# Optimization experiments

Measured on AMD Instinct MI355X. Metric: run time of the kernel, lower is better.

The kernel has to match this reference:

```python
import jax, jax.numpy as jnp
import numpy as np

B, S, D = 2, 2048, 1024
H = 16
DH = D // H  # 64

def setup_inputs() -> dict:
    key = jax.random.key(0)
    ks = jax.random.split(key, 7)
    sc = 1.0 / np.sqrt(DH)
    return {
        "sequences": jax.random.normal(ks[0], (B, S, D), dtype=jnp.float32),
        "Wq": jax.random.normal(ks[1], (H, DH, DH), dtype=jnp.float32) * sc,
        "bq": jax.random.normal(ks[2], (H, DH), dtype=jnp.float32) * 0.02,
        "Wk": jax.random.normal(ks[3], (H, DH, DH), dtype=jnp.float32) * sc,
        "bk": jax.random.normal(ks[4], (H, DH), dtype=jnp.float32) * 0.02,
        "Wv": jax.random.normal(ks[5], (H, DH, DH), dtype=jnp.float32) * sc,
        "bv": jax.random.normal(ks[6], (H, DH), dtype=jnp.float32) * 0.02,
    }

def reference(sequences, Wq, bq, Wk, bk, Wv, bv):
    b, s, _ = sequences.shape
    x = sequences.reshape(b, s, H, DH)  # [B,S,H,Dh]
    # torch Linear: y = x @ W^T + b; W is [out,in] => einsum contracts input dim d
    q = jnp.einsum("bshd,hed->bshe", x, Wq) + bq  # [B,S,H,Dh]
    k = jnp.einsum("bshd,hed->bshe", x, Wk) + bk
    v = jnp.einsum("bshd,hed->bshe", x, Wv) + bv
    scores = jnp.einsum("bshd,bthd->bhst", q, k) / jnp.sqrt(jnp.float32(DH))
    attn = jax.nn.softmax(scores, axis=-1)  # [B,H,S,S]
    out = jnp.einsum("bhst,bthd->bshd", attn, v)  # [B,S,H,Dh]
    return out.reshape(b, s, H * DH)
```

## Files before the change

kernel.cpp:

```cpp
#include <hip/hip_runtime.h>

typedef unsigned short u16;
typedef __bf16 bf16x8 __attribute__((ext_vector_type(8)));
typedef float  f32x4  __attribute__((ext_vector_type(4)));
typedef u16    u16x4  __attribute__((ext_vector_type(4)));

#define HH   16
#define DHH  64
#define SEQL 2048
#define NB   2
#define BHN  (NB * HH)

static __device__ __forceinline__ u16 f2bf(float f) {
    return __builtin_bit_cast(u16, (__bf16)f);
}

static __device__ __forceinline__ void gload_lds16(const void* g, void* l) {
    __builtin_amdgcn_global_load_lds(
        (const __attribute__((address_space(1))) unsigned int*)g,
        (__attribute__((address_space(3))) unsigned int*)l, 16, 0, 0);
}

__global__ __launch_bounds__(256) void wconv_kernel(
    const float* __restrict__ Wq, const float* __restrict__ Wk,
    const float* __restrict__ Wv, u16* __restrict__ Wb)
{
    const int m = blockIdx.y;
    const float* W = (m == 0) ? Wq : (m == 1) ? Wk : Wv;
    const int i = (blockIdx.x * 256 + threadIdx.x) * 4;
    float4 v = *reinterpret_cast<const float4*>(W + i);
    u16x4 o = { f2bf(v.x), f2bf(v.y), f2bf(v.z), f2bf(v.w) };
    *reinterpret_cast<u16x4*>(Wb + (size_t)m * 65536 + i) = o;
}

__global__ __launch_bounds__(256) void qkv_kernel(
    const float* __restrict__ x, const u16* __restrict__ Wb,
    const float* __restrict__ bq, const float* __restrict__ bk,
    const float* __restrict__ bv,
    u16* __restrict__ Qws, u16* __restrict__ Kws, u16* __restrict__ Vtws)
{
    const int h   = blockIdx.y;
    const int r0  = blockIdx.x * 64;
    const int tid = threadIdx.x;
    const int w   = tid >> 6;
    const int l   = tid & 63;
    const int c   = l & 15;
    const int g   = l >> 4;

    __shared__ u16 vt[64 * 72];

    bf16x8 xa[2];
    {
        const float* xp = x + (size_t)(r0 + w * 16 + c) * 1024 + h * 64 + g * 8;
        #pragma unroll
        for (int kh = 0; kh < 2; ++kh) {
            float4 lo = *reinterpret_cast<const float4*>(xp + kh * 32);
            float4 hi = *reinterpret_cast<const float4*>(xp + kh * 32 + 4);
            bf16x8 f;
            f[0]=(__bf16)lo.x; f[1]=(__bf16)lo.y; f[2]=(__bf16)lo.z; f[3]=(__bf16)lo.w;
            f[4]=(__bf16)hi.x; f[5]=(__bf16)hi.y; f[6]=(__bf16)hi.z; f[7]=(__bf16)hi.w;
            xa[kh] = f;
        }
    }

    const int b      = r0 >> 11;
    const int s_base = r0 & (SEQL - 1);
    const int bh     = b * HH + h;

    const float* bs[3] = {bq + h * 64, bk + h * 64, bv + h * 64};

    #pragma unroll
    for (int m = 0; m < 3; ++m) {
        const u16*   W    = Wb + (size_t)m * 65536 + h * 4096;
        const float* bias = bs[m];
        f32x4 acc[4];
        #pragma unroll
        for (int ct = 0; ct < 4; ++ct) {
            acc[ct][0] = 0.f; acc[ct][1] = 0.f; acc[ct][2] = 0.f; acc[ct][3] = 0.f;
        }
        #pragma unroll
        for (int kh = 0; kh < 2; ++kh) {
            #pragma unroll
            for (int ct = 0; ct < 4; ++ct) {
                bf16x8 wf = *reinterpret_cast<const bf16x8*>(
                    W + (ct * 16 + c) * 64 + kh * 32 + g * 8);
                acc[ct] = __builtin_amdgcn_mfma_f32_16x16x32_bf16(xa[kh], wf, acc[ct], 0, 0, 0);
            }
        }
        if (m < 2) {
            u16* outp = (m == 0 ? Qws : Kws) +
                        ((size_t)bh * SEQL + s_base + w * 16 + g * 4) * 64;
            #pragma unroll
            for (int ct = 0; ct < 4; ++ct) {
                float bb = bias[ct * 16 + c];
                #pragma unroll
                for (int r = 0; r < 4; ++r)
                    outp[(size_t)r * 64 + ct * 16 + c] = f2bf(acc[ct][r] + bb);
            }
        } else {
            #pragma unroll
            for (int ct = 0; ct < 4; ++ct) {
                float bb = bias[ct * 16 + c];
                u16x4 pb;
                #pragma unroll
                for (int r = 0; r < 4; ++r)
                    pb[r] = f2bf(acc[ct][r] + bb);
                *reinterpret_cast<u16x4*>(&vt[(ct * 16 + c) * 72 + w * 16 + g * 4]) = pb;
            }
        }
    }
    __syncthreads();
    {
        const int d  = tid >> 2;
        const int s0 = (tid & 3) * 16;
        u16* vp = Vtws + ((size_t)bh * 64 + d) * SEQL + s_base + s0;
        uint4 v0 = *reinterpret_cast<const uint4*>(&vt[d * 72 + s0]);
        uint4 v1 = *reinterpret_cast<const uint4*>(&vt[d * 72 + s0 + 8]);
        *reinterpret_cast<uint4*>(vp)     = v0;
        *reinterpret_cast<uint4*>(vp + 8) = v1;
    }
}

__global__ __launch_bounds__(256) void attn_kernel(
    const u16* __restrict__ Qws, const u16* __restrict__ Kws,
    const u16* __restrict__ Vtws, float* __restrict__ out)
{
    const int p     = blockIdx.x;
    const int lid   = (p & 7) * 64 + (p >> 3);
    const int qtile = lid & 15;
    const int bh    = lid >> 4;
    const int b     = bh >> 4;
    const int h     = bh & 15;

    const int tid = threadIdx.x;
    const int w   = tid >> 6;
    const int l   = tid & 63;
    const int c   = l & 15;
    const int g   = l >> 4;
    const int q0  = qtile * 128 + w * 32;

    __shared__ u16 k_lds[2][64 * 64];
    __shared__ u16 v_lds[2][64 * 64];
    __shared__ u16 plds_all[4 * 32 * 64];
    char* pbase = reinterpret_cast<char*>(plds_all + w * (32 * 64));

    const u16* Kb = Kws  + (size_t)bh * SEQL * 64;
    const u16* Vb = Vtws + (size_t)bh * 64 * SEQL;

    const int rs8 = l >> 3;
    const int sx  = (l & 7) ^ rs8;

    #define STAGE(bb, k0)                                                     \
    {   _Pragma("unroll")                                                     \
        for (int a = 0; a < 2; ++a) {                                         \
            const int rbase = w * 16 + a * 8;                                 \
            const int r     = rbase + rs8;                                    \
            gload_lds16(Kb + (size_t)((k0) + r) * 64 + sx * 8,                \
                        &k_lds[bb][rbase * 64]);                              \
            gload_lds16(Vb + (size_t)r * SEQL + (k0) + sx * 8,                \
                        &v_lds[bb][rbase * 64]);                              \
        }                                                                     \
    }

    bf16x8 qf[2][2];
    #pragma unroll
    for (int qt = 0; qt < 2; ++qt)
        #pragma unroll
        for (int kh = 0; kh < 2; ++kh)
            qf[qt][kh] = *reinterpret_cast<const bf16x8*>(
                Qws + ((size_t)bh * SEQL + q0 + qt * 16 + c) * 64 + kh * 32 + g * 8);

    const f32x4 zero4 = {0.f, 0.f, 0.f, 0.f};
    bf16x8 ones8;
    #pragma unroll
    for (int j = 0; j < 8; ++j) ones8[j] = __builtin_bit_cast(__bf16, (u16)0x3F80);

    f32x4 acc[4][2];
    #pragma unroll
    for (int dt = 0; dt < 4; ++dt)
        #pragma unroll
        for (int qt = 0; qt < 2; ++qt) acc[dt][qt] = zero4;
    float mrow[2] = {-1e30f, -1e30f};
    float lrow[2] = {0.f, 0.f};
    const float SCL = 0.125f * 1.44269504088896340736f;

    const int rdoff = ((g ^ (c & 7)) * 8);

    STAGE(0, 0);
    __syncthreads();

    for (int t = 0; t < SEQL / 64; ++t) {
        const int cur = t & 1;

        if (t + 1 < SEQL / 64) STAGE(cur ^ 1, (t + 1) * 64);

        f32x4 st[4][2];
        __builtin_amdgcn_s_setprio(1);
        #pragma unroll
        for (int kt = 0; kt < 4; ++kt) {
            const int e0 = (kt * 16 + c) * 64 + rdoff;
            bf16x8 ka0 = *reinterpret_cast<const bf16x8*>(&k_lds[cur][e0]);
            bf16x8 ka1 = *reinterpret_cast<const bf16x8*>(&k_lds[cur][e0 ^ 32]);
            #pragma unroll
            for (int qt = 0; qt < 2; ++qt) {
                st[kt][qt] = __builtin_amdgcn_mfma_f32_16x16x32_bf16(ka0, qf[qt][0], zero4,      0, 0, 0);
                st[kt][qt] = __builtin_amdgcn_mfma_f32_16x16x32_bf16(ka1, qf[qt][1], st[kt][qt], 0, 0, 0);
            }
        }
        __builtin_amdgcn_s_setprio(0);

        bf16x8 vf[8];
        #pragma unroll
        for (int dt = 0; dt < 4; ++dt) {
            const int e0 = (dt * 16 + c) * 64 + rdoff;
            vf[dt * 2]     = *reinterpret_cast<const bf16x8*>(&v_lds[cur][e0]);
            vf[dt * 2 + 1] = *reinterpret_cast<const bf16x8*>(&v_lds[cur][e0 ^ 32]);
        }

        #pragma unroll
        for (int qt = 0; qt < 2; ++qt) {
            float a0 = fmaxf(st[0][qt][0], st[0][qt][1]);
            float a1 = fmaxf(st[0][qt][2], st[0][qt][3]);
            float a2 = fmaxf(st[1][qt][0], st[1][qt][1]);
            float a3 = fmaxf(st[1][qt][2], st[1][qt][3]);
            float a4 = fmaxf(st[2][qt][0], st[2][qt][1]);
            float a5 = fmaxf(st[2][qt][2], st[2][qt][3]);
            float a6 = fmaxf(st[3][qt][0], st[3][qt][1]);
            float a7 = fmaxf(st[3][qt][2], st[3][qt][3]);
            float b0 = fmaxf(fmaxf(a0, a1), fmaxf(a2, a3));
            float b1 = fmaxf(fmaxf(a4, a5), fmaxf(a6, a7));
            float mx = fmaxf(b0, b1);
            mx = fmaxf(mx, __shfl_xor(mx, 16, 64));
            mx = fmaxf(mx, __shfl_xor(mx, 32, 64));
            const float mx_s = mx * SCL;

            if (!__all(mx_s <= mrow[qt] + 8.f)) {
                const float mn    = fmaxf(mrow[qt], mx_s);
                const float alpha = __builtin_amdgcn_exp2f(mrow[qt] - mn);
                mrow[qt] = mn;
                lrow[qt] *= alpha;
                #pragma unroll
                for (int dt = 0; dt < 4; ++dt) {
                    acc[dt][qt][0] *= alpha; acc[dt][qt][1] *= alpha;
                    acc[dt][qt][2] *= alpha; acc[dt][qt][3] *= alpha;
                }
            }

            const int row = qt * 16 + c;
            #pragma unroll
            for (int kt = 0; kt < 4; ++kt) {
                u16x4 pb;
                #pragma unroll
                for (int r = 0; r < 4; ++r)
                    pb[r] = f2bf(__builtin_amdgcn_exp2f(fmaf(st[kt][qt][r], SCL, -mrow[qt])));
                const int blk = (kt * 2 + (g >> 1)) ^ (row & 7);
                *reinterpret_cast<u16x4*>(pbase + row * 128 + blk * 16 + (g & 1) * 8) = pb;
            }
        }

        asm volatile("s_waitcnt lgkmcnt(0)" ::: "memory");

        bf16x8 pf[2][2];
        #pragma unroll
        for (int qt = 0; qt < 2; ++qt) {
            const int row = qt * 16 + c;
            #pragma unroll
            for (int kh = 0; kh < 2; ++kh) {
                const int blk = (kh * 4 + g) ^ (row & 7);
                pf[qt][kh] = *reinterpret_cast<const bf16x8*>(pbase + row * 128 + blk * 16);
            }
        }

        __builtin_amdgcn_s_setprio(1);
        #pragma unroll
        for (int dt = 0; dt < 4; ++dt) {
            #pragma unroll
            for (int qt = 0; qt < 2; ++qt) {
                acc[dt][qt] = __builtin_amdgcn_mfma_f32_16x16x32_bf16(vf[dt*2],   pf[qt][0], acc[dt][qt], 0, 0, 0);
                acc[dt][qt] = __builtin_amdgcn_mfma_f32_16x16x32_bf16(vf[dt*2+1], pf[qt][1], acc[dt][qt], 0, 0, 0);
            }
        }
        f32x4 su[2];
        #pragma unroll
        for (int qt = 0; qt < 2; ++qt) {
            su[qt] = __builtin_amdgcn_mfma_f32_16x16x32_bf16(ones8, pf[qt][0], zero4,   0, 0, 0);
            su[qt] = __builtin_amdgcn_mfma_f32_16x16x32_bf16(ones8, pf[qt][1], su[qt], 0, 0, 0);
        }
        __builtin_amdgcn_s_setprio(0);
        lrow[0] += su[0][0];
        lrow[1] += su[1][0];

        __syncthreads();
    }

    const float inv0 = 1.f / lrow[0];
    const float inv1 = 1.f / lrow[1];
    #pragma unroll
    for (int qt = 0; qt < 2; ++qt) {
        const float inv = qt ? inv1 : inv0;
        float* op = out + ((size_t)b * SEQL + q0 + qt * 16 + c) * 1024 + h * 64 + g * 4;
        #pragma unroll
        for (int dt = 0; dt < 4; ++dt) {
            float4 o;
            o.x = acc[dt][qt][0] * inv; o.y = acc[dt][qt][1] * inv;
            o.z = acc[dt][qt][2] * inv; o.w = acc[dt][qt][3] * inv;
            *reinterpret_cast<float4*>(op + dt * 16) = o;
        }
    }
}

extern "C" void kernel_launch(void* const* d_in, const int* in_sizes, int n_in,
                              void* d_out, int out_size, void* d_ws, size_t ws_size,
                              hipStream_t stream) {
    const float* x  = (const float*)d_in[0];
    const float* Wq = (const float*)d_in[1];
    const float* bq = (const float*)d_in[2];
    const float* Wk = (const float*)d_in[3];
    const float* bk = (const float*)d_in[4];
    const float* Wv = (const float*)d_in[5];
    const float* bv = (const float*)d_in[6];
    float* out = (float*)d_out;

    const size_t per = (size_t)BHN * SEQL * 64;
    u16* Qws = (u16*)d_ws;
    u16* Kws = Qws + per;
    u16* Vt  = Kws + per;
    u16* Wb  = Vt  + per;

    wconv_kernel<<<dim3(64, 3), 256, 0, stream>>>(Wq, Wk, Wv, Wb);
    qkv_kernel<<<dim3(64, 16), 256, 0, stream>>>(x, Wb, bq, bk, bv, Qws, Kws, Vt);
    attn_kernel<<<dim3(512), 256, 0, stream>>>(Qws, Kws, Vt, out);
}
```

Baseline: 89.23 us.

## Halve attention query tile to 64 rows per block and double grid

Each wave now handles 16 query rows instead of 32, so a block covers 64 queries and the grid grows from 512 to 1024 blocks. This roughly halves accumulator and score register use and improves load balance and occupancy across the CUs. The cost is that K/V tiles are reloaded from global memory twice as often per query, giving less reuse per LDS stage and more total traffic.

Measured after the change: 92.66 us. 3.8% more time.

```diff
diff --git a/kernel.cpp b/kernel.cpp
--- a/kernel.cpp
+++ b/kernel.cpp
@@ -126,9 +126,9 @@
     const u16* __restrict__ Vtws, float* __restrict__ out)
 {
     const int p     = blockIdx.x;
-    const int lid   = (p & 7) * 64 + (p >> 3);
-    const int qtile = lid & 15;
-    const int bh    = lid >> 4;
+    const int lid   = (p & 7) * 128 + (p >> 3);
+    const int qtile = lid & 31;
+    const int bh    = lid >> 5;
     const int b     = bh >> 4;
     const int h     = bh & 15;
 
@@ -137,12 +137,12 @@
     const int l   = tid & 63;
     const int c   = l & 15;
     const int g   = l >> 4;
-    const int q0  = qtile * 128 + w * 32;
+    const int q0  = qtile * 64 + w * 16;
 
     __shared__ u16 k_lds[2][64 * 64];
     __shared__ u16 v_lds[2][64 * 64];
-    __shared__ u16 plds_all[4 * 32 * 64];
-    char* pbase = reinterpret_cast<char*>(plds_all + w * (32 * 64));
+    __shared__ u16 plds_all[4 * 16 * 64];
+    char* pbase = reinterpret_cast<char*>(plds_all + w * (16 * 64));
 
     const u16* Kb = Kws  + (size_t)bh * SEQL * 64;
     const u16* Vb = Vtws + (size_t)bh * 64 * SEQL;
@@ -162,26 +162,22 @@
         }                                                                     \
     }
 
-    bf16x8 qf[2][2];
-    #pragma unroll
-    for (int qt = 0; qt < 2; ++qt)
-        #pragma unroll
-        for (int kh = 0; kh < 2; ++kh)
-            qf[qt][kh] = *reinterpret_cast<const bf16x8*>(
-                Qws + ((size_t)bh * SEQL + q0 + qt * 16 + c) * 64 + kh * 32 + g * 8);
+    bf16x8 qf[2];
+    #pragma unroll
+    for (int kh = 0; kh < 2; ++kh)
+        qf[kh] = *reinterpret_cast<const bf16x8*>(
+            Qws + ((size_t)bh * SEQL + q0 + c) * 64 + kh * 32 + g * 8);
 
     const f32x4 zero4 = {0.f, 0.f, 0.f, 0.f};
     bf16x8 ones8;
     #pragma unroll
     for (int j = 0; j < 8; ++j) ones8[j] = __builtin_bit_cast(__bf16, (u16)0x3F80);
 
-    f32x4 acc[4][2];
-    #pragma unroll
-    for (int dt = 0; dt < 4; ++dt)
-        #pragma unroll
-        for (int qt = 0; qt < 2; ++qt) acc[dt][qt] = zero4;
-    float mrow[2] = {-1e30f, -1e30f};
-    float lrow[2] = {0.f, 0.f};
+    f32x4 acc[4];
+    #pragma unroll
+    for (int dt = 0; dt < 4; ++dt) acc[dt] = zero4;
+    float mrow = -1e30f;
+    float lrow = 0.f;
     const float SCL = 0.125f * 1.44269504088896340736f;
 
     const int rdoff = ((g ^ (c & 7)) * 8);
@@ -194,18 +190,15 @@
 
         if (t + 1 < SEQL / 64) STAGE(cur ^ 1, (t + 1) * 64);
 
-        f32x4 st[4][2];
+        f32x4 st[4];
         __builtin_amdgcn_s_setprio(1);
         #pragma unroll
         for (int kt = 0; kt < 4; ++kt) {
             const int e0 = (kt * 16 + c) * 64 + rdoff;
             bf16x8 ka0 = *reinterpret_cast<const bf16x8*>(&k_lds[cur][e0]);
             bf16x8 ka1 = *reinterpret_cast<const bf16x8*>(&k_lds[cur][e0 ^ 32]);
-            #pragma unroll
-            for (int qt = 0; qt < 2; ++qt) {
-                st[kt][qt] = __builtin_amdgcn_mfma_f32_16x16x32_bf16(ka0, qf[qt][0], zero4,      0, 0, 0);
-                st[kt][qt] = __builtin_amdgcn_mfma_f32_16x16x32_bf16(ka1, qf[qt][1], st[kt][qt], 0, 0, 0);
-            }
+            st[kt] = __builtin_amdgcn_mfma_f32_16x16x32_bf16(ka0, qf[0], zero4,  0, 0, 0);
+            st[kt] = __builtin_amdgcn_mfma_f32_16x16x32_bf16(ka1, qf[1], st[kt], 0, 0, 0);
         }
         __builtin_amdgcn_s_setprio(0);
 
@@ -217,16 +210,15 @@
             vf[dt * 2 + 1] = *reinterpret_cast<const bf16x8*>(&v_lds[cur][e0 ^ 32]);
         }
 
-        #pragma unroll
-        for (int qt = 0; qt < 2; ++qt) {
-            float a0 = fmaxf(st[0][qt][0], st[0][qt][1]);
-            float a1 = fmaxf(st[0][qt][2], st[0][qt][3]);
-            float a2 = fmaxf(st[1][qt][0], st[1][qt][1]);
-            float a3 = fmaxf(st[1][qt][2], st[1][qt][3]);
-            float a4 = fmaxf(st[2][qt][0], st[2][qt][1]);
-            float a5 = fmaxf(st[2][qt][2], st[2][qt][3]);
-            float a6 = fmaxf(st[3][qt][0], st[3][qt][1]);
-            float a7 = fmaxf(st[3][qt][2], st[3][qt][3]);
+        {
+            float a0 = fmaxf(st[0][0], st[0][1]);
+            float a1 = fmaxf(st[0][2], st[0][3]);
+            float a2 = fmaxf(st[1][0], st[1][1]);
+            float a3 = fmaxf(st[1][2], st[1][3]);
+            float a4 = fmaxf(st[2][0], st[2][1]);
+            float a5 = fmaxf(st[2][2], st[2][3]);
+            float a6 = fmaxf(st[3][0], st[3][1]);
+            float a7 = fmaxf(st[3][2], st[3][3]);
             float b0 = fmaxf(fmaxf(a0, a1), fmaxf(a2, a3));
             float b1 = fmaxf(fmaxf(a4, a5), fmaxf(a6, a7));
             float mx = fmaxf(b0, b1);
@@ -234,78 +226,61 @@
             mx = fmaxf(mx, __shfl_xor(mx, 32, 64));
             const float mx_s = mx * SCL;
 
-            if (!__all(mx_s <= mrow[qt] + 8.f)) {
-                const float mn    = fmaxf(mrow[qt], mx_s);
-                const float alpha = __builtin_amdgcn_exp2f(mrow[qt] - mn);
-                mrow[qt] = mn;
-                lrow[qt] *= alpha;
+            if (!__all(mx_s <= mrow + 8.f)) {
+                const float mn    = fmaxf(mrow, mx_s);
+                const float alpha = __builtin_amdgcn_exp2f(mrow - mn);
+                mrow = mn;
+                lrow *= alpha;
                 #pragma unroll
                 for (int dt = 0; dt < 4; ++dt) {
-                    acc[dt][qt][0] *= alpha; acc[dt][qt][1] *= alpha;
-                    acc[dt][qt][2] *= alpha; acc[dt][qt][3] *= alpha;
+                    acc[dt][0] *= alpha; acc[dt][1] *= alpha;
+                    acc[dt][2] *= alpha; acc[dt][3] *= alpha;
                 }
             }
 
-            const int row = qt * 16 + c;
             #pragma unroll
             for (int kt = 0; kt < 4; ++kt) {
                 u16x4 pb;
                 #pragma unroll
                 for (int r = 0; r < 4; ++r)
-                    pb[r] = f2bf(__builtin_amdgcn_exp2f(fmaf(st[kt][qt][r], SCL, -mrow[qt])));
-                const int blk = (kt * 2 + (g >> 1)) ^ (row & 7);
-                *reinterpret_cast<u16x4*>(pbase + row * 128 + blk * 16 + (g & 1) * 8) = pb;
+                    pb[r] = f2bf(__builtin_amdgcn_exp2f(fmaf(st[kt][r], SCL, -mrow)));
+                const int blk = (kt * 2 + (g >> 1)) ^ (c & 7);
+                *reinterpret_cast<u16x4*>(pbase + c * 128 + blk * 16 + (g & 1) * 8) = pb;
             }
         }
 
         asm volatile("s_waitcnt lgkmcnt(0)" ::: "memory");
 
-        bf16x8 pf[2][2];
-        #pragma unroll
-        for (int qt = 0; qt < 2; ++qt) {
-            const int row = qt * 16 + c;
-            #pragma unroll
-            for (int kh = 0; kh < 2; ++kh) {
-                const int blk = (kh * 4 + g) ^ (row & 7);
-                pf[qt][kh] = *reinterpret_cast<const bf16x8*>(pbase + row * 128 + blk * 16);
-            }
+        bf16x8 pf[2];
+        #pragma unroll
+        for (int kh = 0; kh < 2; ++kh) {
+            const int blk = (kh * 4 + g) ^ (c & 7);
+            pf[kh] = *reinterpret_cast<const bf16x8*>(pbase + c * 128 + blk * 16);
         }
 
         __builtin_amdgcn_s_setprio(1);
         #pragma unroll
         for (int dt = 0; dt < 4; ++dt) {
-            #pragma unroll
-            for (int qt = 0; qt < 2; ++qt) {
-                acc[dt][qt] = __builtin_amdgcn_mfma_f32_16x16x32_bf16(vf[dt*2],   pf[qt][0], acc[dt][qt], 0, 0, 0);
-                acc[dt][qt] = __builtin_amdgcn_mfma_f32_16x16x32_bf16(vf[dt*2+1], pf[qt][1], acc[dt][qt], 0, 0, 0);
-            }
-        }
-        f32x4 su[2];
-        #pragma unroll
-        for (int qt = 0; qt < 2; ++qt) {
-            su[qt] = __builtin_amdgcn_mfma_f32_16x16x32_bf16(ones8, pf[qt][0], zero4,   0, 0, 0);
-            su[qt] = __builtin_amdgcn_mfma_f32_16x16x32_bf16(ones8, pf[qt][1], su[qt], 0, 0, 0);
-        }
+            acc[dt] = __builtin_amdgcn_mfma_f32_16x16x32_bf16(vf[dt*2],   pf[0], acc[dt], 0, 0, 0);
+            acc[dt] = __builtin_amdgcn_mfma_f32_16x16x32_bf16(vf[dt*2+1], pf[1], acc[dt], 0, 0, 0);
+        }
+        f32x4 su;
+        su = __builtin_amdgcn_mfma_f32_16x16x32_bf16(ones8, pf[0], zero4, 0, 0, 0);
+        su = __builtin_amdgcn_mfma_f32_16x16x32_bf16(ones8, pf[1], su,    0, 0, 0);
         __builtin_amdgcn_s_setprio(0);
-        lrow[0] += su[0][0];
-        lrow[1] += su[1][0];
+        lrow += su[0];
 
         __syncthreads();
     }
 
-    const float inv0 = 1.f / lrow[0];
-    const float inv1 = 1.f / lrow[1];
-    #pragma unroll
-    for (int qt = 0; qt < 2; ++qt) {
-        const float inv = qt ? inv1 : inv0;
-        float* op = out + ((size_t)b * SEQL + q0 + qt * 16 + c) * 1024 + h * 64 + g * 4;
-        #pragma unroll
-        for (int dt = 0; dt < 4; ++dt) {
-            float4 o;
-            o.x = acc[dt][qt][0] * inv; o.y = acc[dt][qt][1] * inv;
-            o.z = acc[dt][qt][2] * inv; o.w = acc[dt][qt][3] * inv;
-            *reinterpret_cast<float4*>(op + dt * 16) = o;
-        }
+    const float inv = 1.f / lrow;
+    float* op = out + ((size_t)b * SEQL + q0 + c) * 1024 + h * 64 + g * 4;
+    #pragma unroll
+    for (int dt = 0; dt < 4; ++dt) {
+        float4 o;
+        o.x = acc[dt][0] * inv; o.y = acc[dt][1] * inv;
+        o.z = acc[dt][2] * inv; o.w = acc[dt][3] * inv;
+        *reinterpret_cast<float4*>(op + dt * 16) = o;
     }
 }
 
@@ -329,5 +304,5 @@
 
     wconv_kernel<<<dim3(64, 3), 256, 0, stream>>>(Wq, Wk, Wv, Wb);
     qkv_kernel<<<dim3(64, 16), 256, 0, stream>>>(x, Wb, bq, bk, bv, Qws, Kws, Vt);
-    attn_kernel<<<dim3(512), 256, 0, stream>>>(Qws, Kws, Vt, out);
-}
+    attn_kernel<<<dim3(1024), 256, 0, stream>>>(Qws, Kws, Vt, out);
+}
```

## Software-pipeline PV MFMA behind next QK tile and fold softmax scale into Wq

Applied to the files above, without the earlier changes.

The P·V matrix multiplies for tile t-1 now run right after the QK^T multiplies for tile t. This is done with double-buffered V and P register fragments, so the MFMA unit stays busy while the softmax exponentials of the current tile are computed. The online-softmax rescale and the row-sum update are applied in the right order for the deferred accumulation. Separately, the 1/sqrt(d)·log2(e) factor is folded into the bf16 Wq and bq during conversion, which removes a multiply per score element. The cost is higher register pressure from the duplicated fragments, plus slightly different rounding of the pre-scaled Q.

Measured after the change: 84.98 us. -4.8%, faster.

```diff
diff --git a/kernel.cpp b/kernel.cpp
--- a/kernel.cpp
+++ b/kernel.cpp
@@ -10,6 +10,7 @@
 #define SEQL 2048
 #define NB   2
 #define BHN  (NB * HH)
+#define SCLF 0.1803368801111204f
 
 static __device__ __forceinline__ u16 f2bf(float f) {
     return __builtin_bit_cast(u16, (__bf16)f);
@@ -27,9 +28,10 @@
 {
     const int m = blockIdx.y;
     const float* W = (m == 0) ? Wq : (m == 1) ? Wk : Wv;
+    const float s = (m == 0) ? SCLF : 1.0f;
     const int i = (blockIdx.x * 256 + threadIdx.x) * 4;
     float4 v = *reinterpret_cast<const float4*>(W + i);
-    u16x4 o = { f2bf(v.x), f2bf(v.y), f2bf(v.z), f2bf(v.w) };
+    u16x4 o = { f2bf(v.x * s), f2bf(v.y * s), f2bf(v.z * s), f2bf(v.w * s) };
     *reinterpret_cast<u16x4*>(Wb + (size_t)m * 65536 + i) = o;
 }
 
@@ -73,6 +75,7 @@
     for (int m = 0; m < 3; ++m) {
         const u16*   W    = Wb + (size_t)m * 65536 + h * 4096;
         const float* bias = bs[m];
+        const float  bscl = (m == 0) ? SCLF : 1.0f;
         f32x4 acc[4];
         #pragma unroll
         for (int ct = 0; ct < 4; ++ct) {
@@ -92,7 +95,7 @@
                         ((size_t)bh * SEQL + s_base + w * 16 + g * 4) * 64;
             #pragma unroll
             for (int ct = 0; ct < 4; ++ct) {
-                float bb = bias[ct * 16 + c];
+                float bb = bias[ct * 16 + c] * bscl;
                 #pragma unroll
                 for (int r = 0; r < 4; ++r)
                     outp[(size_t)r * 64 + ct * 16 + c] = f2bf(acc[ct][r] + bb);
@@ -182,14 +185,19 @@
         for (int qt = 0; qt < 2; ++qt) acc[dt][qt] = zero4;
     float mrow[2] = {-1e30f, -1e30f};
     float lrow[2] = {0.f, 0.f};
-    const float SCL = 0.125f * 1.44269504088896340736f;
 
     const int rdoff = ((g ^ (c & 7)) * 8);
+
+    bf16x8 vfA[8], vfB[8];
+    bf16x8 pfA[2][2], pfB[2][2];
+    f32x4  suA[2], suB[2];
 
     STAGE(0, 0);
     __syncthreads();
 
-    for (int t = 0; t < SEQL / 64; ++t) {
+    auto body = [&](bf16x8 (&vfC)[8], bf16x8 (&pfC)[2][2], f32x4 (&suC)[2],
+                    bf16x8 (&vfP)[8], bf16x8 (&pfP)[2][2], f32x4 (&suP)[2],
+                    int t, bool has_prev) {
         const int cur = t & 1;
 
         if (t + 1 < SEQL / 64) STAGE(cur ^ 1, (t + 1) * 64);
@@ -207,18 +215,28 @@
                 st[kt][qt] = __builtin_amdgcn_mfma_f32_16x16x32_bf16(ka1, qf[qt][1], st[kt][qt], 0, 0, 0);
             }
         }
+        if (has_prev) {
+            #pragma unroll
+            for (int dt = 0; dt < 4; ++dt)
+                #pragma unroll
+                for (int qt = 0; qt < 2; ++qt) {
+                    acc[dt][qt] = __builtin_amdgcn_mfma_f32_16x16x32_bf16(vfP[dt*2],   pfP[qt][0], acc[dt][qt], 0, 0, 0);
+                    acc[dt][qt] = __builtin_amdgcn_mfma_f32_16x16x32_bf16(vfP[dt*2+1], pfP[qt][1], acc[dt][qt], 0, 0, 0);
+                }
+        }
         __builtin_amdgcn_s_setprio(0);
 
-        bf16x8 vf[8];
         #pragma unroll
         for (int dt = 0; dt < 4; ++dt) {
             const int e0 = (dt * 16 + c) * 64 + rdoff;
-            vf[dt * 2]     = *reinterpret_cast<const bf16x8*>(&v_lds[cur][e0]);
-            vf[dt * 2 + 1] = *reinterpret_cast<const bf16x8*>(&v_lds[cur][e0 ^ 32]);
+            vfC[dt * 2]     = *reinterpret_cast<const bf16x8*>(&v_lds[cur][e0]);
+            vfC[dt * 2 + 1] = *reinterpret_cast<const bf16x8*>(&v_lds[cur][e0 ^ 32]);
         }
 
         #pragma unroll
         for (int qt = 0; qt < 2; ++qt) {
+            if (has_prev) lrow[qt] += suP[qt][0];
+
             float a0 = fmaxf(st[0][qt][0], st[0][qt][1]);
             float a1 = fmaxf(st[0][qt][2], st[0][qt][3]);
             float a2 = fmaxf(st[1][qt][0], st[1][qt][1]);
@@ -232,10 +250,9 @@
             float mx = fmaxf(b0, b1);
             mx = fmaxf(mx, __shfl_xor(mx, 16, 64));
             mx = fmaxf(mx, __shfl_xor(mx, 32, 64));
-            const float mx_s = mx * SCL;
-
-            if (!__all(mx_s <= mrow[qt] + 8.f)) {
-                const float mn    = fmaxf(mrow[qt], mx_s);
+
+            if (!__all(mx <= mrow[qt] + 8.f)) {
+                const float mn    = fmaxf(mrow[qt], mx);
                 const float alpha = __builtin_amdgcn_exp2f(mrow[qt] - mn);
                 mrow[qt] = mn;
                 lrow[qt] *= alpha;
@@ -252,7 +269,7 @@
                 u16x4 pb;
                 #pragma unroll
                 for (int r = 0; r < 4; ++r)
-                    pb[r] = f2bf(__builtin_amdgcn_exp2f(fmaf(st[kt][qt][r], SCL, -mrow[qt])));
+                    pb[r] = f2bf(__builtin_amdgcn_exp2f(st[kt][qt][r] - mrow[qt]));
                 const int blk = (kt * 2 + (g >> 1)) ^ (row & 7);
                 *reinterpret_cast<u16x4*>(pbase + row * 128 + blk * 16 + (g & 1) * 8) = pb;
             }
@@ -260,38 +277,38 @@
 
         asm volatile("s_waitcnt lgkmcnt(0)" ::: "memory");
 
-        bf16x8 pf[2][2];
         #pragma unroll
         for (int qt = 0; qt < 2; ++qt) {
             const int row = qt * 16 + c;
             #pragma unroll
             for (int kh = 0; kh < 2; ++kh) {
                 const int blk = (kh * 4 + g) ^ (row & 7);
-                pf[qt][kh] = *reinterpret_cast<const bf16x8*>(pbase + row * 128 + blk * 16);
-            }
-        }
-
-        __builtin_amdgcn_s_setprio(1);
-        #pragma unroll
-        for (int dt = 0; dt < 4; ++dt) {
-            #pragma unroll
-            for (int qt = 0; qt < 2; ++qt) {
-                acc[dt][qt] = __builtin_amdgcn_mfma_f32_16x16x32_bf16(vf[dt*2],   pf[qt][0], acc[dt][qt], 0, 0, 0);
-                acc[dt][qt] = __builtin_amdgcn_mfma_f32_16x16x32_bf16(vf[dt*2+1], pf[qt][1], acc[dt][qt], 0, 0, 0);
-            }
-        }
-        f32x4 su[2];
+                pfC[qt][kh] = *reinterpret_cast<const bf16x8*>(pbase + row * 128 + blk * 16);
+            }
+        }
         #pragma unroll
         for (int qt = 0; qt < 2; ++qt) {
-            su[qt] = __builtin_amdgcn_mfma_f32_16x16x32_bf16(ones8, pf[qt][0], zero4,   0, 0, 0);
-            su[qt] = __builtin_amdgcn_mfma_f32_16x16x32_bf16(ones8, pf[qt][1], su[qt], 0, 0, 0);
-        }
-        __builtin_amdgcn_s_setprio(0);
-        lrow[0] += su[0][0];
-        lrow[1] += su[1][0];
+            suC[qt] = __builtin_amdgcn_mfma_f32_16x16x32_bf16(ones8, pfC[qt][0], zero4,   0, 0, 0);
+            suC[qt] = __builtin_amdgcn_mfma_f32_16x16x32_bf16(ones8, pfC[qt][1], suC[qt], 0, 0, 0);
+        }
 
         __syncthreads();
-    }
+    };
+
+    for (int tt = 0; tt < SEQL / 64; tt += 2) {
+        body(vfA, pfA, suA, vfB, pfB, suB, tt,     tt != 0);
+        body(vfB, pfB, suB, vfA, pfA, suA, tt + 1, true);
+    }
+
+    #pragma unroll
+    for (int dt = 0; dt < 4; ++dt)
+        #pragma unroll
+        for (int qt = 0; qt < 2; ++qt) {
+            acc[dt][qt] = __builtin_amdgcn_mfma_f32_16x16x32_bf16(vfB[dt*2],   pfB[qt][0], acc[dt][qt], 0, 0, 0);
+            acc[dt][qt] = __builtin_amdgcn_mfma_f32_16x16x32_bf16(vfB[dt*2+1], pfB[qt][1], acc[dt][qt], 0, 0, 0);
+        }
+    lrow[0] += suB[0][0];
+    lrow[1] += suB[1][0];
 
     const float inv0 = 1.f / lrow[0];
     const float inv1 = 1.f / lrow[1];
```
